# Kernel optimization log

Hardware: AMD Instinct MI355X
Metric: run time of the kernel (lower is better)

## Reference

```python
import jax, jax.numpy as jnp
import numpy as np

B = 4096          # batch of vectors
D = 768           # embedding_size
P = 96            # partition (number of sub-quantizers)
C = 256           # centroids per partition
SD = D // P       # sub-vector dim = 8


def setup_inputs() -> dict:
    key = jax.random.key(0)
    k1, k2 = jax.random.split(key)
    vecs = jax.random.normal(k1, (B, D), dtype=jnp.float32)
    # nn.Parameter(torch.empty(P, C, SD).uniform_(-0.1, 0.1))
    codebook = jax.random.uniform(k2, (P, C, SD), dtype=jnp.float32,
                                  minval=-0.1, maxval=0.1)
    return {"vecs": vecs, "codebook": codebook}


def _quantize(vecs, codebook):
    # vecs: [B, D] -> [B, P, SD]
    v = vecs.reshape(vecs.shape[0], P, SD)
    # proba = -sum((v - c)^2) expanded to avoid the [B,P,C,SD] intermediate:
    # ||v||^2 - 2 v.c + ||c||^2  per (b, p, c)
    v_sq = jnp.sum(v * v, axis=-1, keepdims=True)            # [B, P, 1]
    c_sq = jnp.sum(codebook * codebook, axis=-1)             # [P, C]
    vc = jnp.einsum('bpd,pcd->bpc', v, codebook)             # [B, P, C]
    proba = -(v_sq - 2.0 * vc + c_sq[None])                  # [B, P, C]
    assign = jax.nn.softmax(proba, axis=-1)                  # [B, P, C]
    # straight-through estimator: hard one-hot fwd, soft grad
    index = jnp.argmax(assign, axis=-1)                      # [B, P]
    assign_hard = jax.nn.one_hot(index, C, dtype=assign.dtype)
    assign_ste = jax.lax.stop_gradient(assign_hard - assign) + assign
    # reconstruction: [B,P,C] @ [P,C,SD] -> [B,P,SD] -> [B,D]
    q = jnp.einsum('bpc,pcd->bpd', assign_ste, codebook)
    return q.reshape(vecs.shape[0], -1)


def reference(vecs, codebook):
    return _quantize(vecs, codebook)
```

## Files before the change

kernel.cpp:

```cpp
#include <hip/hip_runtime.h>
#include <cmath>

constexpr int B  = 4096;
constexpr int D  = 768;
constexpr int P  = 96;
constexpr int C  = 256;
constexpr int SD = 8;

__device__ __forceinline__ float tree8(float q0, float q1, float q2, float q3,
                                       float q4, float q5, float q6, float q7)
{
#pragma clang fp contract(off)
    return ((q0 + q1) + (q2 + q3)) + ((q4 + q5) + (q6 + q7));
}

__device__ __forceinline__ float proba_at(const float* __restrict__ cbf,
                                          const float* __restrict__ csq,
                                          int c, float4 va, float4 vb, float vsq)
{
#pragma clang fp contract(off)
    float4 ca = ((const float4*)cbf)[2 * c];
    float4 cb = ((const float4*)cbf)[2 * c + 1];
    float p0 = va.x * ca.x, p1 = va.y * ca.y, p2 = va.z * ca.z, p3 = va.w * ca.w;
    float p4 = vb.x * cb.x, p5 = vb.y * cb.y, p6 = vb.z * cb.z, p7 = vb.w * cb.w;
    float l0 = p0 + p4, l1 = p1 + p5, l2 = p2 + p6, l3 = p3 + p7;
    float vc = (l0 + l2) + (l1 + l3);
    float tt = vsq - 2.0f * vc;
    float u  = tt + csq[c];
    return -u;
}

__global__ __launch_bounds__(256, 2)
void pq_np_emul_kernel(const float* __restrict__ vecs,
                       const float* __restrict__ codebook,
                       float* __restrict__ out)
{
#pragma clang fp contract(off)
    __shared__ float cbf[C * SD];
    __shared__ float csq[C];

    const int p = blockIdx.x;
    const int t = threadIdx.x;
    const int b = blockIdx.y * 256 + t;

    const float4* src = (const float4*)(codebook + (size_t)p * C * SD);
    float4 s0 = src[t];
    float4 s1 = src[t + 256];
    ((float4*)cbf)[t]       = s0;
    ((float4*)cbf)[t + 256] = s1;
    __syncthreads();

    {
        const float* cc = cbf + t * SD;
        float q0 = cc[0]*cc[0], q1 = cc[1]*cc[1], q2 = cc[2]*cc[2], q3 = cc[3]*cc[3];
        float q4 = cc[4]*cc[4], q5 = cc[5]*cc[5], q6 = cc[6]*cc[6], q7 = cc[7]*cc[7];
        csq[t] = tree8(q0,q1,q2,q3,q4,q5,q6,q7);
    }
    __syncthreads();

    const float* vptr = vecs + (size_t)b * D + (size_t)p * SD;
    float4 va = ((const float4*)vptr)[0];
    float4 vb = ((const float4*)vptr)[1];
    float vsq;
    {
        float q0 = va.x*va.x, q1 = va.y*va.y, q2 = va.z*va.z, q3 = va.w*va.w;
        float q4 = vb.x*vb.x, q5 = vb.y*vb.y, q6 = vb.z*vb.z, q7 = vb.w*vb.w;
        vsq = tree8(q0,q1,q2,q3,q4,q5,q6,q7);
    }

    float best = -3.402823466e38f, second = -3.402823466e38f;
    int bi = 0;
    for (int c = 0; c < C; ++c) {
        float pr = proba_at(cbf, csq, c, va, vb, vsq);
        if (pr > best)        { second = best; best = pr; bi = c; }
        else if (pr > second) { second = pr; }
    }
    int idx = bi;

    if (best - second <= 1.0e-6f) {
        float m = best;
        float r0[8] = {0,0,0,0,0,0,0,0};
        float r1[8] = {0,0,0,0,0,0,0,0};
        for (int cg = 0; cg < 16; ++cg) {
            #pragma unroll
            for (int j = 0; j < 8; ++j) {
                float pr = proba_at(cbf, csq, cg * 8 + j, va, vb, vsq);
                r0[j] += expf(pr - m);
            }
        }
        for (int cg = 16; cg < 32; ++cg) {
            #pragma unroll
            for (int j = 0; j < 8; ++j) {
                float pr = proba_at(cbf, csq, cg * 8 + j, va, vb, vsq);
                r1[j] += expf(pr - m);
            }
        }
        float sum = tree8(r0[0],r0[1],r0[2],r0[3],r0[4],r0[5],r0[6],r0[7])
                  + tree8(r1[0],r1[1],r1[2],r1[3],r1[4],r1[5],r1[6],r1[7]);
        float abest = -1.0f;
        int   ai    = 0;
        for (int c = 0; c < C; ++c) {
            float pr = proba_at(cbf, csq, c, va, vb, vsq);
            float e  = expf(pr - m);
            float a  = e / sum;
            if (a > abest) { abest = a; ai = c; }
        }
        idx = ai;
    }

    float4 o0 = ((const float4*)cbf)[2 * idx];
    float4 o1 = ((const float4*)cbf)[2 * idx + 1];
    float4* op = (float4*)(out + (size_t)b * D + (size_t)p * SD);
    op[0] = o0;
    op[1] = o1;
}

extern "C" void kernel_launch(void* const* d_in, const int* in_sizes, int n_in,
                              void* d_out, int out_size, void* d_ws, size_t ws_size,
                              hipStream_t stream)
{
    const float* vecs     = (const float*)d_in[0];
    const float* codebook = (const float*)d_in[1];
    float*       out      = (float*)d_out;

    dim3 grid(P, B / 256);
    dim3 block(256);
    pq_np_emul_kernel<<<grid, block, 0, stream>>>(vecs, codebook, out);
}
```

Measured before the change: 174.4 us.

## Rewrite argmax as FMA dot with half-norm bias and 4-row register blocking

```diff
diff --git a/kernel.cpp b/kernel.cpp
--- a/kernel.cpp
+++ b/kernel.cpp
@@ -7,6 +7,9 @@
 constexpr int C  = 256;
 constexpr int SD = 8;
 
+constexpr int TPB  = 64;
+constexpr int ROWS = 4;
+
 __device__ __forceinline__ float tree8(float q0, float q1, float q2, float q3,
                                        float q4, float q5, float q6, float q7)
 {
@@ -14,7 +17,7 @@
     return ((q0 + q1) + (q2 + q3)) + ((q4 + q5) + (q6 + q7));
 }
 
-__device__ __forceinline__ float proba_at(const float* __restrict__ cbf,
+__device__ __forceinline__ float proba_np(const float* __restrict__ cbf,
                                           const float* __restrict__ csq,
                                           int c, float4 va, float4 vb, float vsq)
 {
@@ -30,48 +33,15 @@
     return -u;
 }
 
-__global__ __launch_bounds__(256, 2)
-void pq_np_emul_kernel(const float* __restrict__ vecs,
-                       const float* __restrict__ codebook,
-                       float* __restrict__ out)
+__device__ __attribute__((noinline))
+int exact_search(const float* __restrict__ cbf, const float* __restrict__ csq,
+                 float4 va, float4 vb, float vsq)
 {
 #pragma clang fp contract(off)
-    __shared__ float cbf[C * SD];
-    __shared__ float csq[C];
-
-    const int p = blockIdx.x;
-    const int t = threadIdx.x;
-    const int b = blockIdx.y * 256 + t;
-
-    const float4* src = (const float4*)(codebook + (size_t)p * C * SD);
-    float4 s0 = src[t];
-    float4 s1 = src[t + 256];
-    ((float4*)cbf)[t]       = s0;
-    ((float4*)cbf)[t + 256] = s1;
-    __syncthreads();
-
-    {
-        const float* cc = cbf + t * SD;
-        float q0 = cc[0]*cc[0], q1 = cc[1]*cc[1], q2 = cc[2]*cc[2], q3 = cc[3]*cc[3];
-        float q4 = cc[4]*cc[4], q5 = cc[5]*cc[5], q6 = cc[6]*cc[6], q7 = cc[7]*cc[7];
-        csq[t] = tree8(q0,q1,q2,q3,q4,q5,q6,q7);
-    }
-    __syncthreads();
-
-    const float* vptr = vecs + (size_t)b * D + (size_t)p * SD;
-    float4 va = ((const float4*)vptr)[0];
-    float4 vb = ((const float4*)vptr)[1];
-    float vsq;
-    {
-        float q0 = va.x*va.x, q1 = va.y*va.y, q2 = va.z*va.z, q3 = va.w*va.w;
-        float q4 = vb.x*vb.x, q5 = vb.y*vb.y, q6 = vb.z*vb.z, q7 = vb.w*vb.w;
-        vsq = tree8(q0,q1,q2,q3,q4,q5,q6,q7);
-    }
-
     float best = -3.402823466e38f, second = -3.402823466e38f;
     int bi = 0;
     for (int c = 0; c < C; ++c) {
-        float pr = proba_at(cbf, csq, c, va, vb, vsq);
+        float pr = proba_np(cbf, csq, c, va, vb, vsq);
         if (pr > best)        { second = best; best = pr; bi = c; }
         else if (pr > second) { second = pr; }
     }
@@ -84,14 +54,14 @@
         for (int cg = 0; cg < 16; ++cg) {
             #pragma unroll
             for (int j = 0; j < 8; ++j) {
-                float pr = proba_at(cbf, csq, cg * 8 + j, va, vb, vsq);
+                float pr = proba_np(cbf, csq, cg * 8 + j, va, vb, vsq);
                 r0[j] += expf(pr - m);
             }
         }
         for (int cg = 16; cg < 32; ++cg) {
             #pragma unroll
             for (int j = 0; j < 8; ++j) {
-                float pr = proba_at(cbf, csq, cg * 8 + j, va, vb, vsq);
+                float pr = proba_np(cbf, csq, cg * 8 + j, va, vb, vsq);
                 r1[j] += expf(pr - m);
             }
         }
@@ -100,19 +70,105 @@
         float abest = -1.0f;
         int   ai    = 0;
         for (int c = 0; c < C; ++c) {
-            float pr = proba_at(cbf, csq, c, va, vb, vsq);
+            float pr = proba_np(cbf, csq, c, va, vb, vsq);
             float e  = expf(pr - m);
             float a  = e / sum;
             if (a > abest) { abest = a; ai = c; }
         }
         idx = ai;
     }
+    return idx;
+}
 
-    float4 o0 = ((const float4*)cbf)[2 * idx];
-    float4 o1 = ((const float4*)cbf)[2 * idx + 1];
-    float4* op = (float4*)(out + (size_t)b * D + (size_t)p * SD);
-    op[0] = o0;
-    op[1] = o1;
+__global__ __launch_bounds__(TPB, 8)
+void pq_fast_kernel(const float* __restrict__ vecs,
+                    const float* __restrict__ codebook,
+                    float* __restrict__ out)
+{
+    __shared__ float cbf [C * SD];
+    __shared__ float csqn[C];
+    __shared__ float csqh[C];
+
+    const int p = blockIdx.x;
+    const int t = threadIdx.x;
+    const int base = blockIdx.y * (TPB * ROWS);
+
+    const float4* src = (const float4*)(codebook + (size_t)p * C * SD);
+    #pragma unroll
+    for (int i = 0; i < 8; ++i)
+        ((float4*)cbf)[t + 64 * i] = src[t + 64 * i];
+    __syncthreads();
+
+    #pragma unroll
+    for (int k = 0; k < 4; ++k) {
+        int c = t + 64 * k;
+        const float* cc = cbf + c * SD;
+        float q0 = cc[0]*cc[0], q1 = cc[1]*cc[1], q2 = cc[2]*cc[2], q3 = cc[3]*cc[3];
+        float q4 = cc[4]*cc[4], q5 = cc[5]*cc[5], q6 = cc[6]*cc[6], q7 = cc[7]*cc[7];
+        float s = tree8(q0,q1,q2,q3,q4,q5,q6,q7);
+        csqn[c] = s;
+        csqh[c] = -0.5f * s;
+    }
+    __syncthreads();
+
+    float4 va[ROWS], vb[ROWS];
+    #pragma unroll
+    for (int r = 0; r < ROWS; ++r) {
+        const float* vptr = vecs + (size_t)(base + 64 * r + t) * D + (size_t)p * SD;
+        va[r] = ((const float4*)vptr)[0];
+        vb[r] = ((const float4*)vptr)[1];
+    }
+
+    float vsq[ROWS];
+    #pragma unroll
+    for (int r = 0; r < ROWS; ++r) {
+        float q0 = va[r].x*va[r].x, q1 = va[r].y*va[r].y,
+              q2 = va[r].z*va[r].z, q3 = va[r].w*va[r].w;
+        float q4 = vb[r].x*vb[r].x, q5 = vb[r].y*vb[r].y,
+              q6 = vb[r].z*vb[r].z, q7 = vb[r].w*vb[r].w;
+        vsq[r] = tree8(q0,q1,q2,q3,q4,q5,q6,q7);
+    }
+
+    float best[ROWS], second[ROWS];
+    int   bi[ROWS];
+    #pragma unroll
+    for (int r = 0; r < ROWS; ++r) {
+        best[r] = -3.402823466e38f; second[r] = -3.402823466e38f; bi[r] = 0;
+    }
+
+    #pragma unroll 2
+    for (int c = 0; c < C; ++c) {
+        float4 ca = ((const float4*)cbf)[2 * c];
+        float4 cb = ((const float4*)cbf)[2 * c + 1];
+        float  ch = csqh[c];
+        #pragma unroll
+        for (int r = 0; r < ROWS; ++r) {
+            float s = fmaf(va[r].x, ca.x, ch);
+            s = fmaf(va[r].y, ca.y, s);
+            s = fmaf(va[r].z, ca.z, s);
+            s = fmaf(va[r].w, ca.w, s);
+            s = fmaf(vb[r].x, cb.x, s);
+            s = fmaf(vb[r].y, cb.y, s);
+            s = fmaf(vb[r].z, cb.z, s);
+            s = fmaf(vb[r].w, cb.w, s);
+            bool gt = s > best[r];
+            second[r] = fmaxf(second[r], fminf(s, best[r]));
+            bi[r]     = gt ? c : bi[r];
+            best[r]   = fmaxf(s, best[r]);
+        }
+    }
+
+    #pragma unroll
+    for (int r = 0; r < ROWS; ++r) {
+        int idx = bi[r];
+        if (best[r] - second[r] <= 2.0e-5f)
+            idx = exact_search(cbf, csqn, va[r], vb[r], vsq[r]);
+        float4 o0 = ((const float4*)cbf)[2 * idx];
+        float4 o1 = ((const float4*)cbf)[2 * idx + 1];
+        float4* op = (float4*)(out + (size_t)(base + 64 * r + t) * D + (size_t)p * SD);
+        op[0] = o0;
+        op[1] = o1;
+    }
 }
 
 extern "C" void kernel_launch(void* const* d_in, const int* in_sizes, int n_in,
@@ -123,7 +179,7 @@
     const float* codebook = (const float*)d_in[1];
     float*       out      = (float*)d_out;
 
-    dim3 grid(P, B / 256);
-    dim3 block(256);
-    pq_np_emul_kernel<<<grid, block, 0, stream>>>(vecs, codebook, out);
+    dim3 grid(P, B / (TPB * ROWS));
+    dim3 block(TPB);
+    pq_fast_kernel<<<grid, block, 0, stream>>>(vecs, codebook, out);
 }
```

Result: slower. 193.9 us (+11.2%).
